# Kernel tuning notes

Hardware: AMD Instinct MI355X
Metric: run time of the kernel (lower is better)

Reference implementation:

```python
import jax, jax.numpy as jnp
import numpy as np

NUM_ITERATIONS = 3


def squash(t, axis=-1):
    # scale * t / sqrt(||t||^2 + eps), scale = ||t||^2 / (1 + ||t||^2)
    sq = jnp.sum(t * t, axis=axis, keepdims=True)
    return (sq / (1.0 + sq)) * t / jnp.sqrt(sq + 1e-8)


def setup_inputs() -> dict:
    key = jax.random.key(0)
    k1, k2 = jax.random.split(key)
    B, C, R, I, O = 128, 10, 8192, 8, 16
    x = jax.random.normal(k1, (B, R, I), dtype=jnp.float32)
    route_weights = jax.random.normal(k2, (C, R, I, O), dtype=jnp.float32) * 0.1
    return {"x": x, "route_weights": route_weights}


def reference(x, route_weights):
    # x: [B, R, I]; route_weights: [C, R, I, O]
    u_hat = jnp.einsum('bri,crio->bcro', x, route_weights)  # [B, C, R, O]
    B, C, R, O = u_hat.shape
    b_ij = jnp.zeros((B, C, R), dtype=u_hat.dtype)
    v_j = None
    for it in range(NUM_ITERATIONS):
        c_ij = jax.nn.softmax(b_ij, axis=1)                 # [B, C, R]
        s_j = jnp.einsum('bcr,bcro->bco', c_ij, u_hat)      # [B, C, O]
        v_j = squash(s_j, axis=-1)                          # [B, C, O]
        if it < NUM_ITERATIONS - 1:
            a_ij = jnp.einsum('bcro,bco->bcr', u_hat, v_j)  # [B, C, R]
            b_ij = b_ij + a_ij
    return v_j
```

## Files before the change

### kernel.cpp

```cpp
#include <hip/hip_runtime.h>
#include <hip/hip_fp16.h>
#include <math.h>

#define B_ 128
#define C_ 10
#define R_ 8192
#define I_ 8
#define O_ 16

typedef __attribute__((ext_vector_type(8))) _Float16 half8;
typedef __attribute__((ext_vector_type(16))) float f32x16;

#define XROW 512
#define WROW 64
#define WZERO 80
#define SBO (C_ * B_ * O_)
#define SLOTS 512
#define NRED 8

__device__ __forceinline__ unsigned pk2(float a, float b) {
    __half2 h = __floats2half2_rn(a, b);
    return *(unsigned*)&h;
}

__global__ __launch_bounds__(512, 4) void fused_iter(const float* __restrict__ x,
                                                     const float* __restrict__ w,
                                                     const float* __restrict__ vsum,
                                                     __half* __restrict__ part,
                                                     int mode) {
    __shared__ unsigned xls[2 * 8 * XROW];
    __shared__ unsigned wls[2 * 81 * WROW];

    const int tid  = threadIdx.x;
    const int wave = tid >> 6;
    const int sg   = wave >> 2;
    const int stid = tid & 255;
    const int lane = tid & 63;
    const int n    = lane & 31;
    const int g    = lane >> 5;
    const int rp_m = (lane & 31) >> 4;
    const int o_m  = lane & 15;
    const int b    = (wave & 3) * 32 + n;
    const int r0   = blockIdx.x * 16 + sg * 8;

    unsigned* const xbase = xls + sg * (8 * XROW);
    unsigned* const wbase = wls + sg * (81 * WROW);
    unsigned* const red_u = xls;

#pragma unroll
    for (int k = 0; k < 8; ++k) {
        const int f = k * 256 + stid;
        const int bb = f >> 4;
        const int rr = (f >> 1) & 7;
        const int q = f & 1;
        const float4 v = *(const float4*)(x + ((size_t)bb * R_ + r0 + rr) * 8 + q * 4);
        *(uint2*)(xbase + rr * XROW + ((bb * 4 + q * 2) ^ (rr << 2))) =
            make_uint2(pk2(v.x, v.y), pk2(v.z, v.w));
    }
#pragma unroll
    for (int k = 0; k < 5; ++k) {
        const int id = k * 256 + stid;
        const int o = id & 15;
        const int r = (id >> 4) & 7;
        const int c = id >> 7;
        const float* wp = w + ((size_t)(c * R_ + r0 + r) * 8) * 16 + o;
        const float f0 = wp[0],  f1 = wp[16],  f2 = wp[32],  f3 = wp[48];
        const float f4 = wp[64], f5 = wp[80],  f6 = wp[96],  f7 = wp[112];
        *(uint4*)(wbase + (c * 8 + r) * WROW + o * 4) =
            make_uint4(pk2(f0, f1), pk2(f2, f3), pk2(f4, f5), pk2(f6, f7));
    }
    if (stid < WROW) wbase[WZERO * WROW + stid] = 0u;
    __syncthreads();

    const int act = (g == rp_m);

    half8 xbr[4];
#pragma unroll
    for (int rp = 0; rp < 4; ++rp) {
        const int row = 2 * rp + g;
        xbr[rp] = *(const half8*)(xbase + row * XROW + ((b * 4) ^ (row << 2)));
    }
    __syncthreads();

#define RED_WRITE_AND_FLUSH(A0,A1,A2,A3,A4,A5,A6,A7)                           \
    {                                                                          \
        const int cp = c & 1;                                                  \
        unsigned* rw = red_u + ((cp * 2 + sg) * 128 + b) * 10;                 \
        *(uint2*)(rw + 2 * g)     = make_uint2(pk2(A0, A1), pk2(A2, A3));      \
        *(uint2*)(rw + 4 + 2 * g) = make_uint2(pk2(A4, A5), pk2(A6, A7));      \
        if (cp == 1) {                                                         \
            __syncthreads();                                                   \
            const int cp2 = tid >> 8, t2 = tid & 255;                          \
            const int b2 = t2 >> 1, oh = t2 & 1;                               \
            const int cout = c - 1 + cp2;                                      \
            const unsigned* r0p = red_u + ((cp2 * 2 + 0) * 128 + b2) * 10 + oh * 4; \
            const unsigned* r1p = red_u + ((cp2 * 2 + 1) * 128 + b2) * 10 + oh * 4; \
            const uint2 xa = *(const uint2*)r0p;                               \
            const uint2 xb2 = *(const uint2*)(r0p + 2);                        \
            const uint2 ya = *(const uint2*)r1p;                               \
            const uint2 yb = *(const uint2*)(r1p + 2);                         \
            unsigned ua[4] = {xa.x, xa.y, xb2.x, xb2.y};                       \
            unsigned ub[4] = {ya.x, ya.y, yb.x, yb.y};                         \
            unsigned uo[4];                                                    \
            _Pragma("unroll")                                                  \
            for (int j = 0; j < 4; ++j) {                                      \
                const float2 fa = __half22float2(*(const __half2*)&ua[j]);     \
                const float2 fb = __half22float2(*(const __half2*)&ub[j]);     \
                uo[j] = pk2(fa.x + fb.x, fa.y + fb.y);                         \
            }                                                                  \
            *(uint4*)(part + ((size_t)blockIdx.x * C_ + cout) * (B_ * O_)      \
                      + b2 * O_ + oh * 8) = make_uint4(uo[0], uo[1], uo[2], uo[3]); \
            __syncthreads();                                                   \
        }                                                                      \
    }

    if (mode) {
        float dinv[4];
        {
            float dacc[4] = {0.f, 0.f, 0.f, 0.f};
#pragma unroll 1
            for (int c = 0; c < C_; ++c) {
                const float4* vp = (const float4*)(vsum + ((size_t)c * B_ + b) * O_ + 4 * g);
                const float4 va = vp[0];
                const float4 vb = vp[2];
#pragma unroll
                for (int rp = 0; rp < 4; ++rp) {
                    const int woff = act ? ((c * 8 + 2 * rp + g) * WROW + o_m * 4)
                                         : (WZERO * WROW);
                    const half8 a = *(const half8*)(wbase + woff);
                    f32x16 u;
#pragma unroll
                    for (int j = 0; j < 16; ++j) u[j] = 0.f;
                    u = __builtin_amdgcn_mfma_f32_32x32x16_f16(a, xbr[rp], u, 0, 0, 0);
                    const float p0 = u[0] * va.x + u[1] * va.y + u[2] * va.z + u[3] * va.w
                                   + u[4] * vb.x + u[5] * vb.y + u[6] * vb.z + u[7] * vb.w;
                    const float p1 = u[8] * va.x + u[9] * va.y + u[10] * va.z + u[11] * va.w
                                   + u[12] * vb.x + u[13] * vb.y + u[14] * vb.z + u[15] * vb.w;
                    const float send = g ? p0 : p1;
                    const float recv = __shfl_xor(send, 32);
                    const float pg = (g ? p1 : p0) + recv;
                    dacc[rp] += __expf(pg);
                }
            }
#pragma unroll
            for (int rp = 0; rp < 4; ++rp) dinv[rp] = 1.0f / dacc[rp];
        }

#pragma unroll 1
        for (int c = 0; c < C_; ++c) {
            const float4* vp = (const float4*)(vsum + ((size_t)c * B_ + b) * O_ + 4 * g);
            const float4 va = vp[0];
            const float4 vb = vp[2];
            float acc[8];
#pragma unroll
            for (int rp = 0; rp < 4; ++rp) {
                const int woff = act ? ((c * 8 + 2 * rp + g) * WROW + o_m * 4)
                                     : (WZERO * WROW);
                const half8 a = *(const half8*)(wbase + woff);
                f32x16 u;
#pragma unroll
                for (int j = 0; j < 16; ++j) u[j] = 0.f;
                u = __builtin_amdgcn_mfma_f32_32x32x16_f16(a, xbr[rp], u, 0, 0, 0);
                const float p0 = u[0] * va.x + u[1] * va.y + u[2] * va.z + u[3] * va.w
                               + u[4] * vb.x + u[5] * vb.y + u[6] * vb.z + u[7] * vb.w;
                const float p1 = u[8] * va.x + u[9] * va.y + u[10] * va.z + u[11] * va.w
                               + u[12] * vb.x + u[13] * vb.y + u[14] * vb.z + u[15] * vb.w;
                const float send = g ? p0 : p1;
                const float recv = __shfl_xor(send, 32);
                const float pg = (g ? p1 : p0) + recv;
                const float w_own = __expf(pg) * dinv[rp];
                const float w_oth = __shfl_xor(w_own, 32);
                const float c0 = g ? w_oth : w_own;
                const float c1 = g ? w_own : w_oth;
                if (rp == 0) {
#pragma unroll
                    for (int j = 0; j < 8; ++j) acc[j] = c0 * u[j] + c1 * u[j + 8];
                } else {
#pragma unroll
                    for (int j = 0; j < 8; ++j) acc[j] += c0 * u[j] + c1 * u[j + 8];
                }
            }
            RED_WRITE_AND_FLUSH(acc[0], acc[1], acc[2], acc[3],
                                acc[4], acc[5], acc[6], acc[7]);
        }
    } else {
#pragma unroll 1
        for (int c = 0; c < C_; ++c) {
            f32x16 acc;
#pragma unroll
            for (int j = 0; j < 16; ++j) acc[j] = 0.f;
#pragma unroll
            for (int rp = 0; rp < 4; ++rp) {
                const int woff = act ? ((c * 8 + 2 * rp + g) * WROW + o_m * 4)
                                     : (WZERO * WROW);
                const half8 a = *(const half8*)(wbase + woff);
                acc = __builtin_amdgcn_mfma_f32_32x32x16_f16(a, xbr[rp], acc, 0, 0, 0);
            }
            const float f0 = (acc[0] + acc[8])  * 0.1f, f1 = (acc[1] + acc[9])  * 0.1f;
            const float f2 = (acc[2] + acc[10]) * 0.1f, f3 = (acc[3] + acc[11]) * 0.1f;
            const float f4 = (acc[4] + acc[12]) * 0.1f, f5 = (acc[5] + acc[13]) * 0.1f;
            const float f6 = (acc[6] + acc[14]) * 0.1f, f7 = (acc[7] + acc[15]) * 0.1f;
            RED_WRITE_AND_FLUSH(f0, f1, f2, f3, f4, f5, f6, f7);
        }
    }
#undef RED_WRITE_AND_FLUSH
}

__global__ __launch_bounds__(256) void reduce1(const __half* __restrict__ part,
                                               float* __restrict__ part2) {
    const int t8 = blockIdx.x * 256 + threadIdx.x;
    const __half* p = part + (size_t)(blockIdx.y * NRED) * SBO + (size_t)t8 * 8;
    float s0 = 0.f, s1 = 0.f, s2 = 0.f, s3 = 0.f;
    float s4 = 0.f, s5 = 0.f, s6 = 0.f, s7 = 0.f;
#pragma unroll
    for (int s = 0; s < NRED; ++s) {
        const uint4 v = *(const uint4*)(p + (size_t)s * SBO);
        const float2 f0 = __half22float2(*(const __half2*)&v.x);
        const float2 f1 = __half22float2(*(const __half2*)&v.y);
        const float2 f2 = __half22float2(*(const __half2*)&v.z);
        const float2 f3 = __half22float2(*(const __half2*)&v.w);
        s0 += f0.x; s1 += f0.y; s2 += f1.x; s3 += f1.y;
        s4 += f2.x; s5 += f2.y; s6 += f3.x; s7 += f3.y;
    }
    float* q = part2 + (size_t)blockIdx.y * SBO + (size_t)t8 * 8;
    *(float4*)q       = make_float4(s0, s1, s2, s3);
    *(float4*)(q + 4) = make_float4(s4, s5, s6, s7);
}

__global__ __launch_bounds__(256) void finish_pass(const float* __restrict__ part2,
                                                   float* __restrict__ vsum,
                                                   float* __restrict__ out,
                                                   int mode) {
    const int t = blockIdx.x * 256 + threadIdx.x;
    float sum = 0.f;
#pragma unroll 8
    for (int s = 0; s < SLOTS / NRED; ++s)
        sum += part2[(size_t)s * SBO + t];

    float sq = sum * sum;
    sq += __shfl_xor(sq, 1);
    sq += __shfl_xor(sq, 2);
    sq += __shfl_xor(sq, 4);
    sq += __shfl_xor(sq, 8);
    const float scale = sq / ((1.0f + sq) * sqrtf(sq + 1e-8f));
    const float v = scale * sum;

    if (mode == 0) {
        vsum[t] = v;
    } else if (mode == 1) {
        vsum[t] += v;
    } else {
        const int o = t & 15, b = (t >> 4) & 127, c = t >> 11;
        out[((size_t)b * C_ + c) * O_ + o] = v;
    }
}

extern "C" void kernel_launch(void* const* d_in, const int* in_sizes, int n_in,
                              void* d_out, int out_size, void* d_ws, size_t ws_size,
                              hipStream_t stream) {
    const float* x = (const float*)d_in[0];
    const float* w = (const float*)d_in[1];
    float* out = (float*)d_out;

    __half* part = (__half*)d_ws;
    float* part2 = (float*)(part + (size_t)SLOTS * SBO);
    float* vsum  = part2 + (size_t)(SLOTS / NRED) * SBO;

    const dim3 fgrid(R_ / 16);
    const dim3 rgrid(10, SLOTS / NRED);
    const dim3 ggrid(80);

    for (int it = 0; it < 3; ++it) {
        const int mode = (it > 0);
        const int fmode = (it == 2) ? 2 : it;
        fused_iter<<<fgrid, 512, 0, stream>>>(x, w, vsum, part, mode);
        reduce1<<<rgrid, 256, 0, stream>>>(part, part2);
        finish_pass<<<ggrid, 256, 0, stream>>>(part2, vsum, out, fmode);
    }
}
```

Before: 217.0 us.

## Fuse two-stage partial reduction into one finish kernel and share zero accumulator

Replaces the reduce1 + finish_pass kernel pair with a single finish_fused kernel. It reads the 512 fp16 partial slots directly, reduces them through shared memory and applies squash in the same launch. This removes one launch per iteration and the fp32 intermediate buffer's write and read traffic. It also feeds a shared zero vector into the MFMA accumulator instead of zeroing it each time. The new kernel reads 4-byte elements strided by slot, which may coalesce less well than the old 16-byte loads.

New measurement: 203.7 us. -6.1%, faster.

```diff
diff --git a/kernel.cpp b/kernel.cpp
--- a/kernel.cpp
+++ b/kernel.cpp
@@ -16,7 +16,6 @@
 #define WZERO 80
 #define SBO (C_ * B_ * O_)
 #define SLOTS 512
-#define NRED 8
 
 __device__ __forceinline__ unsigned pk2(float a, float b) {
     __half2 h = __floats2half2_rn(a, b);
@@ -81,6 +80,10 @@
         xbr[rp] = *(const half8*)(xbase + row * XROW + ((b * 4) ^ (row << 2)));
     }
     __syncthreads();
+
+    f32x16 zero16;
+#pragma unroll
+    for (int j = 0; j < 16; ++j) zero16[j] = 0.f;
 
 #define RED_WRITE_AND_FLUSH(A0,A1,A2,A3,A4,A5,A6,A7)                           \
     {                                                                          \
@@ -128,10 +131,7 @@
                     const int woff = act ? ((c * 8 + 2 * rp + g) * WROW + o_m * 4)
                                          : (WZERO * WROW);
                     const half8 a = *(const half8*)(wbase + woff);
-                    f32x16 u;
-#pragma unroll
-                    for (int j = 0; j < 16; ++j) u[j] = 0.f;
-                    u = __builtin_amdgcn_mfma_f32_32x32x16_f16(a, xbr[rp], u, 0, 0, 0);
+                    const f32x16 u = __builtin_amdgcn_mfma_f32_32x32x16_f16(a, xbr[rp], zero16, 0, 0, 0);
                     const float p0 = u[0] * va.x + u[1] * va.y + u[2] * va.z + u[3] * va.w
                                    + u[4] * vb.x + u[5] * vb.y + u[6] * vb.z + u[7] * vb.w;
                     const float p1 = u[8] * va.x + u[9] * va.y + u[10] * va.z + u[11] * va.w
@@ -157,10 +157,7 @@
                 const int woff = act ? ((c * 8 + 2 * rp + g) * WROW + o_m * 4)
                                      : (WZERO * WROW);
                 const half8 a = *(const half8*)(wbase + woff);
-                f32x16 u;
-#pragma unroll
-                for (int j = 0; j < 16; ++j) u[j] = 0.f;
-                u = __builtin_amdgcn_mfma_f32_32x32x16_f16(a, xbr[rp], u, 0, 0, 0);
+                const f32x16 u = __builtin_amdgcn_mfma_f32_32x32x16_f16(a, xbr[rp], zero16, 0, 0, 0);
                 const float p0 = u[0] * va.x + u[1] * va.y + u[2] * va.z + u[3] * va.w
                                + u[4] * vb.x + u[5] * vb.y + u[6] * vb.z + u[7] * vb.w;
                 const float p1 = u[8] * va.x + u[9] * va.y + u[10] * va.z + u[11] * va.w
@@ -188,13 +185,12 @@
         for (int c = 0; c < C_; ++c) {
             f32x16 acc;
 #pragma unroll
-            for (int j = 0; j < 16; ++j) acc[j] = 0.f;
-#pragma unroll
             for (int rp = 0; rp < 4; ++rp) {
                 const int woff = act ? ((c * 8 + 2 * rp + g) * WROW + o_m * 4)
                                      : (WZERO * WROW);
                 const half8 a = *(const half8*)(wbase + woff);
-                acc = __builtin_amdgcn_mfma_f32_32x32x16_f16(a, xbr[rp], acc, 0, 0, 0);
+                acc = __builtin_amdgcn_mfma_f32_32x32x16_f16(a, xbr[rp],
+                                                             rp == 0 ? zero16 : acc, 0, 0, 0);
             }
             const float f0 = (acc[0] + acc[8])  * 0.1f, f1 = (acc[1] + acc[9])  * 0.1f;
             const float f2 = (acc[2] + acc[10]) * 0.1f, f3 = (acc[3] + acc[11]) * 0.1f;
@@ -206,52 +202,48 @@
 #undef RED_WRITE_AND_FLUSH
 }
 
-__global__ __launch_bounds__(256) void reduce1(const __half* __restrict__ part,
-                                               float* __restrict__ part2) {
-    const int t8 = blockIdx.x * 256 + threadIdx.x;
-    const __half* p = part + (size_t)(blockIdx.y * NRED) * SBO + (size_t)t8 * 8;
-    float s0 = 0.f, s1 = 0.f, s2 = 0.f, s3 = 0.f;
-    float s4 = 0.f, s5 = 0.f, s6 = 0.f, s7 = 0.f;
-#pragma unroll
-    for (int s = 0; s < NRED; ++s) {
-        const uint4 v = *(const uint4*)(p + (size_t)s * SBO);
-        const float2 f0 = __half22float2(*(const __half2*)&v.x);
-        const float2 f1 = __half22float2(*(const __half2*)&v.y);
-        const float2 f2 = __half22float2(*(const __half2*)&v.z);
-        const float2 f3 = __half22float2(*(const __half2*)&v.w);
-        s0 += f0.x; s1 += f0.y; s2 += f1.x; s3 += f1.y;
-        s4 += f2.x; s5 += f2.y; s6 += f3.x; s7 += f3.y;
-    }
-    float* q = part2 + (size_t)blockIdx.y * SBO + (size_t)t8 * 8;
-    *(float4*)q       = make_float4(s0, s1, s2, s3);
-    *(float4*)(q + 4) = make_float4(s4, s5, s6, s7);
-}
-
-__global__ __launch_bounds__(256) void finish_pass(const float* __restrict__ part2,
-                                                   float* __restrict__ vsum,
-                                                   float* __restrict__ out,
-                                                   int mode) {
-    const int t = blockIdx.x * 256 + threadIdx.x;
-    float sum = 0.f;
+__global__ __launch_bounds__(512) void finish_fused(const __half* __restrict__ part,
+                                                    float* __restrict__ vsum,
+                                                    float* __restrict__ out,
+                                                    int mode) {
+    __shared__ float2 red[16][32];
+    const int q  = threadIdx.x >> 5;
+    const int pp = threadIdx.x & 31;
+    const int pi = blockIdx.x * 32 + pp;
+
+    const unsigned* pu = (const unsigned*)part + (size_t)q * 32 * (SBO / 2) + pi;
+    float sx = 0.f, sy = 0.f;
 #pragma unroll 8
-    for (int s = 0; s < SLOTS / NRED; ++s)
-        sum += part2[(size_t)s * SBO + t];
-
-    float sq = sum * sum;
-    sq += __shfl_xor(sq, 1);
-    sq += __shfl_xor(sq, 2);
-    sq += __shfl_xor(sq, 4);
-    sq += __shfl_xor(sq, 8);
-    const float scale = sq / ((1.0f + sq) * sqrtf(sq + 1e-8f));
-    const float v = scale * sum;
-
-    if (mode == 0) {
-        vsum[t] = v;
-    } else if (mode == 1) {
-        vsum[t] += v;
-    } else {
-        const int o = t & 15, b = (t >> 4) & 127, c = t >> 11;
-        out[((size_t)b * C_ + c) * O_ + o] = v;
+    for (int s = 0; s < 32; ++s) {
+        const unsigned uv = pu[(size_t)s * (SBO / 2)];
+        const float2 f = __half22float2(*(const __half2*)&uv);
+        sx += f.x; sy += f.y;
+    }
+    red[q][pp] = make_float2(sx, sy);
+    __syncthreads();
+
+    if (threadIdx.x < 32) {
+        float2 s2 = red[0][pp];
+#pragma unroll
+        for (int j = 1; j < 16; ++j) { s2.x += red[j][pp].x; s2.y += red[j][pp].y; }
+
+        float sq = s2.x * s2.x + s2.y * s2.y;
+        sq += __shfl_xor(sq, 1);
+        sq += __shfl_xor(sq, 2);
+        sq += __shfl_xor(sq, 4);
+        const float scale = sq / ((1.0f + sq) * sqrtf(sq + 1e-8f));
+        const float v0 = scale * s2.x, v1 = scale * s2.y;
+        const int t0 = 2 * pi;
+
+        if (mode == 0) {
+            *(float2*)(vsum + t0) = make_float2(v0, v1);
+        } else if (mode == 1) {
+            const float2 old = *(const float2*)(vsum + t0);
+            *(float2*)(vsum + t0) = make_float2(old.x + v0, old.y + v1);
+        } else {
+            const int o = t0 & 15, b = (t0 >> 4) & 127, c = t0 >> 11;
+            *(float2*)(out + ((size_t)b * C_ + c) * O_ + o) = make_float2(v0, v1);
+        }
     }
 }
 
@@ -263,18 +255,15 @@
     float* out = (float*)d_out;
 
     __half* part = (__half*)d_ws;
-    float* part2 = (float*)(part + (size_t)SLOTS * SBO);
-    float* vsum  = part2 + (size_t)(SLOTS / NRED) * SBO;
+    float* vsum  = (float*)(part + (size_t)SLOTS * SBO);
 
     const dim3 fgrid(R_ / 16);
-    const dim3 rgrid(10, SLOTS / NRED);
-    const dim3 ggrid(80);
+    const dim3 ggrid(320);
 
     for (int it = 0; it < 3; ++it) {
         const int mode = (it > 0);
         const int fmode = (it == 2) ? 2 : it;
         fused_iter<<<fgrid, 512, 0, stream>>>(x, w, vsum, part, mode);
-        reduce1<<<rgrid, 256, 0, stream>>>(part, part2);
-        finish_pass<<<ggrid, 256, 0, stream>>>(part2, vsum, out, fmode);
-    }
-}
+        finish_fused<<<ggrid, 512, 0, stream>>>(part, vsum, out, fmode);
+    }
+}
```
